# Optimization experiments

Measured on AMD Instinct MI355X. Metric: run time of the kernel, lower is better.

Reference implementation:

```python
import jax, jax.numpy as jnp
import numpy as np

EPS = 1e-5
K = 20
MAXV = 64


def knn_idx(x, k):
    # x: [B,N,D] -> idx: [B,N,k] (excluding self, matching torch topk of -dist)
    xx = jnp.sum(x * x, axis=-1, keepdims=True)                      # [B,N,1]
    dist = xx - 2.0 * jnp.einsum('bnd,bmd->bnm', x, x) + jnp.swapaxes(xx, 1, 2)
    _, idx = jax.lax.top_k(-dist, k + 1)
    return idx[:, :, 1:]


def edge_conv(x, W, gamma, beta, mean, var, k):
    # x: [B,N,C]; W: [O,2C]; BN in eval mode; max over k neighbors
    idx = knn_idx(x, k)                                              # [B,N,k]
    nbr = jax.vmap(lambda xi, ii: xi[ii])(x, idx)                    # [B,N,k,C]
    ctr = jnp.broadcast_to(x[:, :, None, :], nbr.shape)
    ef = jnp.concatenate([ctr, nbr - ctr], axis=-1)                  # [B,N,k,2C]
    y = jnp.einsum('bnkc,oc->bnko', ef, W)                           # 1x1 conv
    y = (y - mean) * (gamma * jax.lax.rsqrt(var + EPS)) + beta       # BN eval
    y = jnp.where(y >= 0, y, 0.2 * y)                                # LeakyReLU
    return jnp.max(y, axis=2)                                        # [B,N,O]


def setup_inputs() -> dict:
    key = jax.random.key(0)
    ks = jax.random.split(key, 32)
    f32 = jnp.float32
    def w(k_, o, i):
        return jax.random.normal(k_, (o, i), f32) / np.float32(np.sqrt(i))
    def vec(k_, c):
        return jax.random.normal(k_, (c,), f32) * 0.1
    d = {}
    d['x'] = jax.random.normal(ks[0], (4, 8192, 5), f32)
    # EdgeConv 1: 5 -> 32
    d['W1'] = w(ks[1], 32, 10)
    d['g1'] = jax.random.uniform(ks[2], (32,), f32, 0.5, 1.5)
    d['b1'] = vec(ks[3], 32); d['m1'] = vec(ks[4], 32)
    d['v1'] = jax.random.uniform(ks[5], (32,), f32, 0.5, 1.5)
    # EdgeConv 2: 32 -> 64
    d['W2'] = w(ks[6], 64, 64)
    d['g2'] = jax.random.uniform(ks[7], (64,), f32, 0.5, 1.5)
    d['b2'] = vec(ks[8], 64); d['m2'] = vec(ks[9], 64)
    d['v2'] = jax.random.uniform(ks[10], (64,), f32, 0.5, 1.5)
    # EdgeConv 3: 64 -> 128
    d['W3'] = w(ks[11], 128, 128)
    d['g3'] = jax.random.uniform(ks[12], (128,), f32, 0.5, 1.5)
    d['b3'] = vec(ks[13], 128); d['m3'] = vec(ks[14], 128)
    d['v3'] = jax.random.uniform(ks[15], (128,), f32, 0.5, 1.5)
    # conv_global: 224 -> 256
    d['Wg'] = w(ks[16], 256, 224)
    d['gg'] = jax.random.uniform(ks[17], (256,), f32, 0.5, 1.5)
    d['bg'] = vec(ks[18], 256); d['mg'] = vec(ks[19], 256)
    d['vg'] = jax.random.uniform(ks[20], (256,), f32, 0.5, 1.5)
    # vertex predictor heads
    d['Wv1'] = w(ks[21], 512, 256); d['bv1'] = vec(ks[22], 512)
    d['Wv2'] = w(ks[23], 192, 512); d['bv2'] = vec(ks[24], 192)
    d['Wq1'] = w(ks[25], 64, 256); d['bq1'] = vec(ks[26], 64)
    d['Wq2'] = w(ks[27], 1, 64); d['bq2'] = vec(ks[28], 1)
    return d


def reference(x, W1, g1, b1, m1, v1, W2, g2, b2, m2, v2, W3, g3, b3, m3, v3,
              Wg, gg, bg, mg, vg, Wv1, bv1, Wv2, bv2, Wq1, bq1, Wq2, bq2):
    B = x.shape[0]
    x1 = edge_conv(x, W1, g1, b1, m1, v1, K)      # [B,N,32]
    x2 = edge_conv(x1, W2, g2, b2, m2, v2, K)     # [B,N,64]
    x3 = edge_conv(x2, W3, g3, b3, m3, v3, K)     # [B,N,128]
    x_concat = jnp.concatenate([x1, x2, x3], axis=2)               # [B,N,224]
    xg = jnp.einsum('bnc,oc->bno', x_concat, Wg)                   # 1x1 conv1d
    xg = (xg - mg) * (gg * jax.lax.rsqrt(vg + EPS)) + bg
    xg = jnp.where(xg >= 0, xg, 0.2 * xg)
    gfeat = jnp.max(xg, axis=1)                                    # [B,256]
    h = jax.nn.relu(gfeat @ Wv1.T + bv1)                           # Dropout=eval id
    vertex_coords = (h @ Wv2.T + bv2).reshape(B, MAXV, 3)
    q = jax.nn.relu(gfeat @ Wq1.T + bq1)
    nvs = jax.nn.sigmoid(q @ Wq2.T + bq2)                          # [B,1]
    num_vertices = jnp.clip(jnp.round(nvs * MAXV), 1, MAXV).astype(jnp.int32)
    return (vertex_coords, num_vertices[:, 0], nvs[:, 0], gfeat, x_concat)
```

## Files before the change

kernel.cpp:

```cpp
#include <hip/hip_runtime.h>
#include <hip/hip_bf16.h>


#define NPTS 8192
#define BATCH 4
#define KNBR 20

template <int D, int RS, int S, int TJ>
__global__ __launch_bounds__(128) void knn_part(
    const float* feat, float* xcat) {
    __shared__ float xj[TJ * D];
    __shared__ float xxj[TJ];
    const int JC = NPTS / S;

    int gi = blockIdx.x * 128 + threadIdx.x;
    int s  = blockIdx.y;
    int b  = gi >> 13;
    int ib = gi & (NPTS - 1);
    const float* fb = feat + (size_t)b * NPTS * RS;

    float xi[D];
    if (D % 4 == 0) {
        #pragma unroll
        for (int c4 = 0; c4 < D / 4; ++c4) {
            float4 v = *(const float4*)(fb + (size_t)ib * RS + 4 * c4);
            xi[4 * c4] = v.x; xi[4 * c4 + 1] = v.y;
            xi[4 * c4 + 2] = v.z; xi[4 * c4 + 3] = v.w;
        }
    } else {
        #pragma unroll
        for (int c = 0; c < D; ++c) xi[c] = fb[(size_t)ib * RS + c];
    }
    float xxi = 0.f;
    #pragma unroll
    for (int c = 0; c < D; ++c) xxi = fmaf(xi[c], xi[c], xxi);

    float dl[21];
    int   il[21];
    #pragma unroll
    for (int t = 0; t < 21; ++t) { dl[t] = __builtin_inff(); il[t] = 0; }

    for (int j0 = s * JC; j0 < (s + 1) * JC; j0 += TJ) {
        __syncthreads();
        if (D % 4 == 0) {
            for (int e = threadIdx.x; e < TJ * (D / 4); e += 128) {
                int r = e / (D / 4), c4 = e % (D / 4);
                float4 v = *(const float4*)(fb + (size_t)(j0 + r) * RS + 4 * c4);
                *(float4*)(xj + r * D + 4 * c4) = v;
            }
        } else {
            for (int e = threadIdx.x; e < TJ * D; e += 128) {
                int r = e / D, c = e % D;
                xj[e] = fb[(size_t)(j0 + r) * RS + c];
            }
        }
        if (threadIdx.x < TJ) {
            const float* row = fb + (size_t)(j0 + threadIdx.x) * RS;
            float sm = 0.f;
            if (D % 4 == 0) {
                #pragma unroll
                for (int c4 = 0; c4 < D / 4; ++c4) {
                    float4 v = *(const float4*)(row + 4 * c4);
                    sm = fmaf(v.x, v.x, sm); sm = fmaf(v.y, v.y, sm);
                    sm = fmaf(v.z, v.z, sm); sm = fmaf(v.w, v.w, sm);
                }
            } else {
                #pragma unroll
                for (int c = 0; c < D; ++c) sm = fmaf(row[c], row[c], sm);
            }
            xxj[threadIdx.x] = sm;
        }
        __syncthreads();
        for (int jj = 0; jj < TJ; ++jj) {
            float dot = 0.f;
            if (D % 4 == 0) {
                const float* xr = xj + jj * D;
                #pragma unroll
                for (int c4 = 0; c4 < D / 4; ++c4) {
                    float4 v = *(const float4*)(xr + 4 * c4);
                    dot = fmaf(xi[4 * c4 + 0], v.x, dot);
                    dot = fmaf(xi[4 * c4 + 1], v.y, dot);
                    dot = fmaf(xi[4 * c4 + 2], v.z, dot);
                    dot = fmaf(xi[4 * c4 + 3], v.w, dot);
                }
            } else {
                #pragma unroll
                for (int c = 0; c < D; ++c) dot = fmaf(xi[c], xj[jj * D + c], dot);
            }
            float d = __builtin_fmaf(-2.f, dot, xxi + xxj[jj]);
            if (d < dl[20]) {
                dl[20] = d; il[20] = j0 + jj;
                #pragma unroll
                for (int t = 20; t > 0; --t) {
                    if (dl[t] < dl[t - 1]) {
                        float td = dl[t]; dl[t] = dl[t - 1]; dl[t - 1] = td;
                        int   ti = il[t]; il[t] = il[t - 1]; il[t - 1] = ti;
                    }
                }
            }
        }
    }
    unsigned short* cp =
        (unsigned short*)(xcat + (size_t)gi * 224 + 96) + s * 21;
    #pragma unroll
    for (int t = 0; t < 21; ++t) cp[t] = (unsigned short)il[t];
}

template <int D, int RS, int S>
__global__ __launch_bounds__(256) void knn_merge(
    const float* feat, const float* xcat, unsigned short* __restrict__ idxout) {
    int gi = blockIdx.x * 256 + threadIdx.x;
    int b  = gi >> 13;
    int ib = gi & (NPTS - 1);
    const float* fb = feat + (size_t)b * NPTS * RS;

    float xi[D];
    if (D % 4 == 0) {
        #pragma unroll
        for (int c4 = 0; c4 < D / 4; ++c4) {
            float4 v = *(const float4*)(fb + (size_t)ib * RS + 4 * c4);
            xi[4 * c4] = v.x; xi[4 * c4 + 1] = v.y;
            xi[4 * c4 + 2] = v.z; xi[4 * c4 + 3] = v.w;
        }
    } else {
        #pragma unroll
        for (int c = 0; c < D; ++c) xi[c] = fb[(size_t)ib * RS + c];
    }
    float xxi = 0.f;
    #pragma unroll
    for (int c = 0; c < D; ++c) xxi = fmaf(xi[c], xi[c], xxi);

    const unsigned short* cp =
        (const unsigned short*)(xcat + (size_t)gi * 224 + 96);

    float dl[21];
    int   il[21];
    #pragma unroll
    for (int t = 0; t < 21; ++t) { dl[t] = __builtin_inff(); il[t] = 0; }

    for (int t = 0; t < S * 21; ++t) {
        int j = ((int)cp[t]) & (NPTS - 1);
        const float* row = fb + (size_t)j * RS;
        float dot = 0.f, xx = 0.f;
        if (D % 4 == 0) {
            #pragma unroll
            for (int c4 = 0; c4 < D / 4; ++c4) {
                float4 v = *(const float4*)(row + 4 * c4);
                dot = fmaf(xi[4 * c4], v.x, dot);     xx = fmaf(v.x, v.x, xx);
                dot = fmaf(xi[4 * c4 + 1], v.y, dot); xx = fmaf(v.y, v.y, xx);
                dot = fmaf(xi[4 * c4 + 2], v.z, dot); xx = fmaf(v.z, v.z, xx);
                dot = fmaf(xi[4 * c4 + 3], v.w, dot); xx = fmaf(v.w, v.w, xx);
            }
        } else {
            #pragma unroll
            for (int c = 0; c < D; ++c) {
                float v = row[c];
                dot = fmaf(xi[c], v, dot);
                xx  = fmaf(v, v, xx);
            }
        }
        float d = __builtin_fmaf(-2.f, dot, xxi + xx);
        if (d < dl[20]) {
            dl[20] = d; il[20] = j;
            #pragma unroll
            for (int u = 20; u > 0; --u) {
                if (dl[u] < dl[u - 1]) {
                    float td = dl[u]; dl[u] = dl[u - 1]; dl[u - 1] = td;
                    int   ti = il[u]; il[u] = il[u - 1]; il[u - 1] = ti;
                }
            }
        }
    }
    unsigned short* op = idxout + (size_t)gi * KNBR;
    #pragma unroll
    for (int t = 1; t < 21; ++t) op[t - 1] = (unsigned short)il[t];
}

template <int CIN, int RS, int COUT, int OTILE, int P>
__global__ __launch_bounds__(256) void edgeconv_kernel(
    const float* feat, const unsigned short* __restrict__ knn,
    const float* __restrict__ W, const float* __restrict__ g,
    const float* __restrict__ beta, const float* __restrict__ mu,
    const float* __restrict__ var,
    float* outb, int concat_off) {
    __shared__ float diff[P][KNBR][CIN];
    __shared__ float xil[P][CIN];
    __shared__ unsigned short kidx[P * KNBR];
    __shared__ float sl[OTILE], bl[OTILE], ml[OTILE];

    int tid = threadIdx.x;
    int h   = blockIdx.y;
    int n0  = blockIdx.x * P;
    int b   = n0 >> 13;
    const float* fbase = feat + ((size_t)b << 13) * RS;

    for (int e = tid; e < P * CIN; e += 256)
        xil[e / CIN][e % CIN] = feat[(size_t)(n0 + e / CIN) * RS + e % CIN];
    for (int e = tid; e < P * KNBR; e += 256)
        kidx[e] = knn[(size_t)(n0 + e / KNBR) * KNBR + e % KNBR] & (NPTS - 1);
    for (int e = tid; e < OTILE; e += 256) {
        int o = h * OTILE + e;
        sl[e] = g[o] * rsqrtf(var[o] + 1e-5f);
        bl[e] = beta[o];
        ml[e] = mu[o];
    }
    __syncthreads();

    if (CIN % 4 == 0) {
        for (int e = tid; e < P * KNBR * (CIN / 4); e += 256) {
            int r = e / (CIN / 4), c4 = e % (CIN / 4);
            int p = r / KNBR, k = r % KNBR;
            int j = (int)kidx[r];
            float4 v = *(const float4*)(fbase + (size_t)j * RS + 4 * c4);
            diff[p][k][4 * c4 + 0] = v.x - xil[p][4 * c4 + 0];
            diff[p][k][4 * c4 + 1] = v.y - xil[p][4 * c4 + 1];
            diff[p][k][4 * c4 + 2] = v.z - xil[p][4 * c4 + 2];
            diff[p][k][4 * c4 + 3] = v.w - xil[p][4 * c4 + 3];
        }
    } else {
        for (int e = tid; e < P * KNBR * CIN; e += 256) {
            int r = e / CIN, c = e % CIN;
            int p = r / CIN == 0 ? 0 : 0;
            int pp = r / KNBR, k = r % KNBR;
            int j = (int)kidx[r];
            diff[pp][k][c] = fbase[(size_t)j * RS + c] - xil[pp][c];
        }
    }
    __syncthreads();

    int ol = tid % OTILE, p = tid / OTILE;
    int o  = h * OTILE + ol;

    float wreg[CIN];
    #pragma unroll
    for (int c = 0; c < CIN; ++c) wreg[c] = W[(size_t)o * (2 * CIN) + c];
    float a = 0.f;
    #pragma unroll
    for (int c = 0; c < CIN; ++c) a = fmaf(wreg[c], xil[p][c], a);
    #pragma unroll
    for (int c = 0; c < CIN; ++c) wreg[c] = W[(size_t)o * (2 * CIN) + CIN + c];

    float s = sl[ol], mm = ml[ol], bb = bl[ol];
    float best = -__builtin_inff();
    for (int k = 0; k < KNBR; ++k) {
        float ac0 = a, ac1 = 0.f, ac2 = 0.f, ac3 = 0.f;
        #pragma unroll
        for (int c = 0; c < CIN; ++c) {
            float d = diff[p][k][c];
            if ((c & 3) == 0)      ac0 = fmaf(wreg[c], d, ac0);
            else if ((c & 3) == 1) ac1 = fmaf(wreg[c], d, ac1);
            else if ((c & 3) == 2) ac2 = fmaf(wreg[c], d, ac2);
            else                   ac3 = fmaf(wreg[c], d, ac3);
        }
        float acc = ((ac0 + ac1) + ac2) + ac3;
        float y = (acc - mm) * s + bb;
        y = (y >= 0.f) ? y : 0.2f * y;
        best = fmaxf(best, y);
    }
    outb[(size_t)(n0 + p) * 224 + concat_off + o] = best;
}

__global__ __launch_bounds__(256) void convglobal_kernel(
    const float* __restrict__ xcat,
    const float* __restrict__ Wg, const float* __restrict__ gg,
    const float* __restrict__ bg, const float* __restrict__ mg,
    const float* __restrict__ vg,
    float* __restrict__ partial) {
    const int KC = 56, PT = 64, OT = 64, ST = 68;
    __shared__ float flT[KC * ST];
    __shared__ float WlT[KC * ST];
    __shared__ float red[64 * 17];

    int tid = threadIdx.x;
    int oi  = tid & 15, pi = tid >> 4;
    int o0  = blockIdx.y * OT;
    int n0  = blockIdx.x * PT;
    int b   = n0 >> 13;
    int pchunk = blockIdx.x & 127;

    float acc[4][4];
    #pragma unroll
    for (int u = 0; u < 4; ++u)
        #pragma unroll
        for (int v = 0; v < 4; ++v) acc[u][v] = 0.f;

    for (int kc = 0; kc < 224; kc += KC) {
        __syncthreads();
        for (int e = tid; e < PT * (KC / 4); e += 256) {
            int p = e / (KC / 4), c4 = e % (KC / 4);
            float4 v = *(const float4*)(xcat + (size_t)(n0 + p) * 224 + kc + 4 * c4);
            flT[(4 * c4 + 0) * ST + p] = v.x;
            flT[(4 * c4 + 1) * ST + p] = v.y;
            flT[(4 * c4 + 2) * ST + p] = v.z;
            flT[(4 * c4 + 3) * ST + p] = v.w;
        }
        for (int e = tid; e < OT * (KC / 4); e += 256) {
            int o = e / (KC / 4), c4 = e % (KC / 4);
            float4 v = *(const float4*)(Wg + (size_t)(o0 + o) * 224 + kc + 4 * c4);
            WlT[(4 * c4 + 0) * ST + o] = v.x;
            WlT[(4 * c4 + 1) * ST + o] = v.y;
            WlT[(4 * c4 + 2) * ST + o] = v.z;
            WlT[(4 * c4 + 3) * ST + o] = v.w;
        }
        __syncthreads();
        #pragma unroll 8
        for (int c = 0; c < KC; ++c) {
            float4 w4 = *(const float4*)(WlT + c * ST + oi * 4);
            float4 f4 = *(const float4*)(flT + c * ST + pi * 4);
            acc[0][0] = fmaf(w4.x, f4.x, acc[0][0]);
            acc[0][1] = fmaf(w4.x, f4.y, acc[0][1]);
            acc[0][2] = fmaf(w4.x, f4.z, acc[0][2]);
            acc[0][3] = fmaf(w4.x, f4.w, acc[0][3]);
            acc[1][0] = fmaf(w4.y, f4.x, acc[1][0]);
            acc[1][1] = fmaf(w4.y, f4.y, acc[1][1]);
            acc[1][2] = fmaf(w4.y, f4.z, acc[1][2]);
            acc[1][3] = fmaf(w4.y, f4.w, acc[1][3]);
            acc[2][0] = fmaf(w4.z, f4.x, acc[2][0]);
            acc[2][1] = fmaf(w4.z, f4.y, acc[2][1]);
            acc[2][2] = fmaf(w4.z, f4.z, acc[2][2]);
            acc[2][3] = fmaf(w4.z, f4.w, acc[2][3]);
            acc[3][0] = fmaf(w4.w, f4.x, acc[3][0]);
            acc[3][1] = fmaf(w4.w, f4.y, acc[3][1]);
            acc[3][2] = fmaf(w4.w, f4.z, acc[3][2]);
            acc[3][3] = fmaf(w4.w, f4.w, acc[3][3]);
        }
    }
    #pragma unroll
    for (int u = 0; u < 4; ++u) {
        int oL = oi * 4 + u, o = o0 + oL;
        float s = gg[o] * rsqrtf(vg[o] + 1e-5f);
        float mm = mg[o], bb = bg[o];
        float best = -__builtin_inff();
        #pragma unroll
        for (int v = 0; v < 4; ++v) {
            float y = (acc[u][v] - mm) * s + bb;
            y = (y >= 0.f) ? y : 0.2f * y;
            best = fmaxf(best, y);
        }
        red[oL * 17 + pi] = best;
    }
    __syncthreads();
    if (tid < 64) {
        float best = -__builtin_inff();
        #pragma unroll
        for (int q = 0; q < 16; ++q) best = fmaxf(best, red[tid * 17 + q]);
        partial[((size_t)(b * 128 + pchunk)) * 256 + o0 + tid] = best;
    }
}

__global__ void reduce_gfeat_kernel(const float* __restrict__ partial,
                                    float* __restrict__ gfeat,
                                    float* __restrict__ outg) {
    int b = blockIdx.x, o = threadIdx.x;
    float best = -__builtin_inff();
    for (int ch = 0; ch < 128; ++ch)
        best = fmaxf(best, partial[((size_t)b * 128 + ch) * 256 + o]);
    gfeat[b * 256 + o] = best;
    outg[b * 256 + o]  = best;
}

__global__ __launch_bounds__(256) void heads_kernel(
    const float* __restrict__ gfeat,
    const float* __restrict__ Wv1, const float* __restrict__ bv1,
    const float* __restrict__ Wv2, const float* __restrict__ bv2,
    const float* __restrict__ Wq1, const float* __restrict__ bq1,
    const float* __restrict__ Wq2, const float* __restrict__ bq2,
    float* __restrict__ out) {
    int b = blockIdx.x, t = threadIdx.x;
    __shared__ float gf[256], h[512], q[64];
    gf[t] = gfeat[b * 256 + t];
    __syncthreads();
    for (int r = t; r < 512; r += 256) {
        float acc = bv1[r];
        for (int c = 0; c < 256; ++c) acc = fmaf(Wv1[r * 256 + c], gf[c], acc);
        h[r] = fmaxf(acc, 0.f);
    }
    __syncthreads();
    if (t < 192) {
        float acc = bv2[t];
        for (int c = 0; c < 512; ++c) acc = fmaf(Wv2[t * 512 + c], h[c], acc);
        out[b * 192 + t] = acc;
    } else {
        int r = t - 192;
        if (r < 64) {
            float acc = bq1[r];
            for (int c = 0; c < 256; ++c) acc = fmaf(Wq1[r * 256 + c], gf[c], acc);
            q[r] = fmaxf(acc, 0.f);
        }
    }
    __syncthreads();
    if (t == 0) {
        float acc = bq2[0];
        for (int c = 0; c < 64; ++c) acc = fmaf(Wq2[c], q[c], acc);
        float nv = 1.0f / (1.0f + expf(-acc));
        out[772 + b] = nv;
        float num = fminf(fmaxf(rintf(nv * 64.0f), 1.0f), 64.0f);
        out[768 + b] = num;
    }
}

extern "C" void kernel_launch(void* const* d_in, const int* in_sizes, int n_in,
                              void* d_out, int out_size, void* d_ws, size_t ws_size,
                              hipStream_t stream) {
    (void)in_sizes; (void)n_in; (void)out_size; (void)ws_size;
    const float* x   = (const float*)d_in[0];
    const float* W1  = (const float*)d_in[1];
    const float* g1  = (const float*)d_in[2];
    const float* b1  = (const float*)d_in[3];
    const float* m1  = (const float*)d_in[4];
    const float* v1  = (const float*)d_in[5];
    const float* W2  = (const float*)d_in[6];
    const float* g2  = (const float*)d_in[7];
    const float* b2  = (const float*)d_in[8];
    const float* m2  = (const float*)d_in[9];
    const float* v2  = (const float*)d_in[10];
    const float* W3  = (const float*)d_in[11];
    const float* g3  = (const float*)d_in[12];
    const float* b3  = (const float*)d_in[13];
    const float* m3  = (const float*)d_in[14];
    const float* v3  = (const float*)d_in[15];
    const float* Wg  = (const float*)d_in[16];
    const float* gg  = (const float*)d_in[17];
    const float* bg  = (const float*)d_in[18];
    const float* mg  = (const float*)d_in[19];
    const float* vg  = (const float*)d_in[20];
    const float* Wv1 = (const float*)d_in[21];
    const float* bv1 = (const float*)d_in[22];
    const float* Wv2 = (const float*)d_in[23];
    const float* bv2 = (const float*)d_in[24];
    const float* Wq1 = (const float*)d_in[25];
    const float* bq1 = (const float*)d_in[26];
    const float* Wq2 = (const float*)d_in[27];
    const float* bq2 = (const float*)d_in[28];

    float* out  = (float*)d_out;
    float* xcat = out + 1800;
    char* ws = (char*)d_ws;
    const int ROWS = BATCH * NPTS;

    unsigned short* idx  = (unsigned short*)(ws);
    float*          part = (float*)(ws);
    float*          gft  = (float*)(ws + 524288);

    knn_part<5, 5, 8, 128><<<dim3(ROWS / 128, 8), 128, 0, stream>>>(x, xcat);
    knn_merge<5, 5, 8><<<ROWS / 256, 256, 0, stream>>>(x, xcat, idx);
    edgeconv_kernel<5, 5, 32, 32, 8>
        <<<dim3(ROWS / 8, 1), 256, 0, stream>>>(x, idx, W1, g1, b1, m1, v1, xcat, 0);

    knn_part<32, 224, 8, 128><<<dim3(ROWS / 128, 8), 128, 0, stream>>>(xcat, xcat);
    knn_merge<32, 224, 8><<<ROWS / 256, 256, 0, stream>>>(xcat, xcat, idx);
    edgeconv_kernel<32, 224, 64, 64, 4>
        <<<dim3(ROWS / 4, 1), 256, 0, stream>>>(xcat, idx, W2, g2, b2, m2, v2, xcat, 32);

    knn_part<64, 224, 8, 64><<<dim3(ROWS / 128, 8), 128, 0, stream>>>(xcat + 32, xcat);
    knn_merge<64, 224, 8><<<ROWS / 256, 256, 0, stream>>>(xcat + 32, xcat, idx);
    edgeconv_kernel<64, 224, 128, 64, 4>
        <<<dim3(ROWS / 4, 2), 256, 0, stream>>>(xcat + 32, idx, W3, g3, b3, m3, v3, xcat, 96);

    convglobal_kernel<<<dim3(ROWS / 64, 4), 256, 0, stream>>>(
        xcat, Wg, gg, bg, mg, vg, part);
    reduce_gfeat_kernel<<<BATCH, 256, 0, stream>>>(part, gft, out + 776);

    heads_kernel<<<BATCH, 256, 0, stream>>>(
        gft, Wv1, bv1, Wv2, bv2, Wq1, bq1, Wq2, bq2, out);
}
```

Measured before the change: 4.369 ms.

## Buffer kNN candidates in LDS and batch sorted-list insertions per wave

The kNN partial kernel no longer runs the 21-element insertion sort the moment a candidate beats the current worst. Candidates below a cached threshold are appended to a small per-thread LDS buffer, and the whole wave flushes its buffers together once any lane's buffer is full. This cuts warp divergence from scattered per-lane insertions, at the cost of LDS traffic, a stale threshold that lets extra candidates through, and a ballot check on every candidate.

```diff
diff --git a/kernel.cpp b/kernel.cpp
--- a/kernel.cpp
+++ b/kernel.cpp
@@ -6,11 +6,12 @@
 #define BATCH 4
 #define KNBR 20
 
-template <int D, int RS, int S, int TJ>
+template <int D, int RS, int S, int TJ, int B>
 __global__ __launch_bounds__(128) void knn_part(
     const float* feat, float* xcat) {
     __shared__ float xj[TJ * D];
     __shared__ float xxj[TJ];
+    __shared__ uint2 buf[128 * B];
     const int JC = NPTS / S;
 
     int gi = blockIdx.x * 128 + threadIdx.x;
@@ -18,6 +19,7 @@
     int b  = gi >> 13;
     int ib = gi & (NPTS - 1);
     const float* fb = feat + (size_t)b * NPTS * RS;
+    uint2* mybuf = buf + threadIdx.x * B;
 
     float xi[D];
     if (D % 4 == 0) {
@@ -39,6 +41,9 @@
     int   il[21];
     #pragma unroll
     for (int t = 0; t < 21; ++t) { dl[t] = __builtin_inff(); il[t] = 0; }
+
+    float thr = __builtin_inff();
+    int   cnt = 0;
 
     for (int j0 = s * JC; j0 < (s + 1) * JC; j0 += TJ) {
         __syncthreads();
@@ -88,8 +93,38 @@
                 for (int c = 0; c < D; ++c) dot = fmaf(xi[c], xj[jj * D + c], dot);
             }
             float d = __builtin_fmaf(-2.f, dot, xxi + xxj[jj]);
-            if (d < dl[20]) {
-                dl[20] = d; il[20] = j0 + jj;
+            if (__any(cnt == B)) {
+                for (int u = 0; u < B; ++u) {
+                    if (u < cnt) {
+                        uint2 pk = mybuf[u];
+                        float dd = __uint_as_float(pk.x);
+                        if (dd < dl[20]) {
+                            dl[20] = dd; il[20] = (int)pk.y;
+                            #pragma unroll
+                            for (int t = 20; t > 0; --t) {
+                                if (dl[t] < dl[t - 1]) {
+                                    float td = dl[t]; dl[t] = dl[t - 1]; dl[t - 1] = td;
+                                    int   ti = il[t]; il[t] = il[t - 1]; il[t - 1] = ti;
+                                }
+                            }
+                        }
+                    }
+                }
+                cnt = 0;
+                thr = dl[20];
+            }
+            if (d < thr) {
+                mybuf[cnt] = make_uint2(__float_as_uint(d), (unsigned)(j0 + jj));
+                ++cnt;
+            }
+        }
+    }
+    for (int u = 0; u < B; ++u) {
+        if (u < cnt) {
+            uint2 pk = mybuf[u];
+            float dd = __uint_as_float(pk.x);
+            if (dd < dl[20]) {
+                dl[20] = dd; il[20] = (int)pk.y;
                 #pragma unroll
                 for (int t = 20; t > 0; --t) {
                     if (dl[t] < dl[t - 1]) {
@@ -220,7 +255,6 @@
     } else {
         for (int e = tid; e < P * KNBR * CIN; e += 256) {
             int r = e / CIN, c = e % CIN;
-            int p = r / CIN == 0 ? 0 : 0;
             int pp = r / KNBR, k = r % KNBR;
             int j = (int)kidx[r];
             diff[pp][k][c] = fbase[(size_t)j * RS + c] - xil[pp][c];
@@ -442,17 +476,17 @@
     float*          part = (float*)(ws);
     float*          gft  = (float*)(ws + 524288);
 
-    knn_part<5, 5, 8, 128><<<dim3(ROWS / 128, 8), 128, 0, stream>>>(x, xcat);
+    knn_part<5, 5, 8, 128, 8><<<dim3(ROWS / 128, 8), 128, 0, stream>>>(x, xcat);
     knn_merge<5, 5, 8><<<ROWS / 256, 256, 0, stream>>>(x, xcat, idx);
     edgeconv_kernel<5, 5, 32, 32, 8>
         <<<dim3(ROWS / 8, 1), 256, 0, stream>>>(x, idx, W1, g1, b1, m1, v1, xcat, 0);
 
-    knn_part<32, 224, 8, 128><<<dim3(ROWS / 128, 8), 128, 0, stream>>>(xcat, xcat);
+    knn_part<32, 224, 8, 128, 8><<<dim3(ROWS / 128, 8), 128, 0, stream>>>(xcat, xcat);
     knn_merge<32, 224, 8><<<ROWS / 256, 256, 0, stream>>>(xcat, xcat, idx);
     edgeconv_kernel<32, 224, 64, 64, 4>
         <<<dim3(ROWS / 4, 1), 256, 0, stream>>>(xcat, idx, W2, g2, b2, m2, v2, xcat, 32);
 
-    knn_part<64, 224, 8, 64><<<dim3(ROWS / 128, 8), 128, 0, stream>>>(xcat + 32, xcat);
+    knn_part<64, 224, 8, 64, 8><<<dim3(ROWS / 128, 8), 128, 0, stream>>>(xcat + 32, xcat);
     knn_merge<64, 224, 8><<<ROWS / 256, 256, 0, stream>>>(xcat + 32, xcat, idx);
     edgeconv_kernel<64, 224, 128, 64, 4>
         <<<dim3(ROWS / 4, 2), 256, 0, stream>>>(xcat + 32, idx, W3, g3, b3, m3, v3, xcat, 96);
```

Measured after the change: 3.833 ms. -12.3%, faster.
